# Kernel optimization log

Measured on AMD Instinct MI355X. Metric: run time of the kernel, lower is better.

## Reference

```python
import jax, jax.numpy as jnp
import numpy as np

NUM_NODES = 50000
NUM_RELATIONS = 16
HIDDEN = 128
NUM_LAYERS = 3
NUM_EDGES = 1600000


def setup_inputs() -> dict:
    key = jax.random.key(0)
    ks = jax.random.split(key, 6)
    edge_index = jax.random.randint(ks[0], (2, NUM_EDGES), 0, NUM_NODES, dtype=jnp.int64)
    edge_type = jax.random.randint(ks[1], (NUM_EDGES,), 0, NUM_RELATIONS, dtype=jnp.int64)
    scale = 1.0 / np.sqrt(HIDDEN)
    node_init = jax.random.normal(ks[2], (NUM_NODES, HIDDEN), dtype=jnp.float32) * scale
    W = jax.random.normal(ks[3], (NUM_LAYERS, NUM_RELATIONS, HIDDEN, HIDDEN), dtype=jnp.float32) * scale
    root = jax.random.normal(ks[4], (NUM_LAYERS, HIDDEN, HIDDEN), dtype=jnp.float32) * scale
    bias = jnp.zeros((NUM_LAYERS, HIDDEN), dtype=jnp.float32)
    return {"edge_index": edge_index, "edge_type": edge_type,
            "node_init": node_init, "W": W, "root": root, "bias": bias}


def _fast_rgcn_layer(x, src, tgt, edge_type, W_r, root_r, bias_r):
    # FastRGCNConv with aggr='mean': mean of messages per (target node, relation),
    # message = x_src @ W[relation]. By linearity, aggregate normalized x_src per
    # (node, relation) first, then apply relation weights with a single einsum.
    N, d = x.shape
    R = W_r.shape[0]
    seg = tgt * R + edge_type                       # combined (node, relation) segment id
    msg = x[src]                                    # [E, d] irregular gather
    agg = jax.ops.segment_sum(msg, seg, num_segments=N * R).reshape(N, R, d)
    cnt = jax.ops.segment_sum(jnp.ones_like(edge_type, dtype=x.dtype), seg,
                              num_segments=N * R).reshape(N, R, 1)
    agg = agg / jnp.clip(cnt, 1.0, None)            # per-(node,relation) mean
    out = jnp.einsum('nrd,rdo->no', agg, W_r)       # relation-specific transform
    out = out + x @ root_r + bias_r                 # root/self connection + bias
    return out


def reference(edge_index, edge_type, node_init, W, root, bias):
    src, tgt = edge_index[0], edge_index[1]
    x = node_init
    for i in range(NUM_LAYERS):
        x = _fast_rgcn_layer(x, src, tgt, edge_type, W[i], root[i], bias[i])
        if i < NUM_LAYERS - 1:
            x = jax.nn.relu(x)  # dropout omitted (eval mode)
    return x
```

## Files before the change

kernel.cpp:

```cpp
#include <hip/hip_runtime.h>
#include <hip/hip_bf16.h>

#define N_NODES   50000
#define N_REL     16
#define HID       128
#define N_EDGES   1600000
#define N_TILES   3125
#define N_BINS    800000
#define N_RUNS    50000
#define N_SCANBLK 49
#define N_MBLK    1563
#define PAYLOAD_CAP 2400064
#define BS_LAYER  278528
#define AG_STRIDE 136

typedef unsigned short ushort_t;
typedef __attribute__((ext_vector_type(8))) short short8;
typedef __attribute__((ext_vector_type(4))) float f32x4;

union BF2U { __hip_bfloat162 h; unsigned u; };

__device__ __forceinline__ unsigned pack_bf16_2(float x, float y) {
  BF2U c; c.h = __float22bfloat162_rn(make_float2(x, y));
  return c.u;
}

__device__ __forceinline__ void lds_barrier() {
  asm volatile("s_waitcnt lgkmcnt(0)\n\ts_barrier" ::: "memory");
}


__global__ __launch_bounds__(256) void k_hist(const int* __restrict__ ei,
                                              const int* __restrict__ et,
                                              int* __restrict__ cnt,
                                              int* __restrict__ rank) {
  int e = blockIdx.x * 256 + threadIdx.x;
  int tgt = ei[N_EDGES + e];
  int r   = et[e];
  int key = ((tgt >> 4) << 8) | (r << 4) | (tgt & 15);
  rank[e] = atomicAdd(&cnt[key], 1);
}

__global__ __launch_bounds__(256) void k_runpad(const int* __restrict__ cnt,
                                                int* __restrict__ padtot) {
  int r = blockIdx.x * 256 + threadIdx.x;
  if (r >= N_RUNS) return;
  const int4* c4 = (const int4*)(cnt + r * 16);
  int s = 0;
#pragma unroll
  for (int j = 0; j < 4; ++j) { int4 v = c4[j]; s += v.x + v.y + v.z + v.w; }
  padtot[r] = (s + 15) & ~15;
}

__global__ __launch_bounds__(256) void k_btot(const int* __restrict__ in,
                                              int* __restrict__ totals, int n) {
  __shared__ int s[256];
  int t = threadIdx.x, b = blockIdx.x;
  int sum = 0;
  for (int j = 0; j < 4; ++j) {
    int idx = b * 1024 + j * 256 + t;
    sum += (idx < n) ? in[idx] : 0;
  }
  s[t] = sum; __syncthreads();
  for (int ofs = 128; ofs > 0; ofs >>= 1) {
    if (t < ofs) s[t] += s[t + ofs];
    __syncthreads();
  }
  if (t == 0) totals[b] = s[0];
}

__global__ __launch_bounds__(1024) void k_scan_totals(int* totals, int* endp, int nblk) {
  __shared__ int s[1024];
  int t = threadIdx.x;
  int v = (t < nblk) ? totals[t] : 0;
  s[t] = v; __syncthreads();
  for (int ofs = 1; ofs < 1024; ofs <<= 1) {
    int x = (t >= ofs) ? s[t - ofs] : 0;
    __syncthreads();
    s[t] += x;
    __syncthreads();
  }
  if (t < nblk) totals[t] = s[t] - v;
  if (t == nblk - 1) *endp = s[t];
}

__global__ __launch_bounds__(1024) void k_scan_within(int* __restrict__ a,
                                                      const int* __restrict__ totals,
                                                      int n) {
  __shared__ int s[1024];
  int t = threadIdx.x, blk = blockIdx.x;
  int b = blk * 1024 + t;
  int v = (b < n) ? a[b] : 0;
  s[t] = v; __syncthreads();
  for (int ofs = 1; ofs < 1024; ofs <<= 1) {
    int x = (t >= ofs) ? s[t - ofs] : 0;
    __syncthreads();
    s[t] += x;
    __syncthreads();
  }
  if (b < n) a[b] = totals[blk] + s[t] - v;
}

__global__ __launch_bounds__(256) void k_fineoff(const int* __restrict__ cnt,
                                                 const int* __restrict__ run_start,
                                                 int* __restrict__ fine_start,
                                                 unsigned* __restrict__ payload) {
  int r = blockIdx.x * 256 + threadIdx.x;
  if (r >= N_RUNS) return;
  int base = run_start[r];
  int e1   = run_start[r + 1];
  int pfx = 0;
  for (int i = 0; i < 16; ++i) {
    fine_start[r * 16 + i] = base + pfx;
    pfx += cnt[r * 16 + i];
  }
  const unsigned dummy = ((unsigned)N_NODES << 16) | (1u << 4) | 15u;
  for (int j = base + pfx; j < e1; ++j) payload[j] = dummy;
}

__global__ __launch_bounds__(256) void k_sort(const int* __restrict__ ei,
                                              const int* __restrict__ et,
                                              const int* __restrict__ cnt,
                                              const int* __restrict__ fine_start,
                                              const int* __restrict__ rank,
                                              unsigned* __restrict__ payload) {
  int e = blockIdx.x * 256 + threadIdx.x;
  int src = ei[e];
  int tgt = ei[N_EDGES + e];
  int r   = et[e];
  int key = ((tgt >> 4) << 8) | (r << 4) | (tgt & 15);
  int c = cnt[key]; c = c > 4095 ? 4095 : c;
  int pos = fine_start[key] + rank[e];
  payload[pos] = ((unsigned)src << 16) | ((unsigned)c << 4) | (unsigned)(tgt & 15);
}

__global__ __launch_bounds__(256) void k_bt(const float* __restrict__ W,
                                            const float* __restrict__ root,
                                            ushort_t* __restrict__ Bs) {
  int idx = blockIdx.x * 256 + threadIdx.x;
  int lane = idx & 63;
  int fl   = idx >> 6;
  int frag = fl % 544;
  int l    = fl / 544;
  int cb = frag & 7, kk = (frag >> 3) & 3, r = frag >> 5;
  int col = cb * 16 + (lane & 15);
  int d0  = kk * 32 + (lane >> 4) * 8;
  const float* srcp = (r < 16)
      ? W + ((size_t)(l * N_REL + r) * HID + d0) * HID + col
      : root + ((size_t)l * HID + d0) * HID + col;
  ushort_t out[8];
#pragma unroll
  for (int j = 0; j < 8; ++j) {
    union { __hip_bfloat16 h; ushort_t u; } c;
    c.h = __float2bfloat16(srcp[(size_t)j * HID]);
    out[j] = c.u;
  }
  *(short8*)(Bs + ((size_t)fl << 9) + lane * 8) = *(short8*)out;
}

__global__ __launch_bounds__(256) void k_xh(const float* __restrict__ xin,
                                            ushort_t* __restrict__ xh) {
  int i = blockIdx.x * 256 + threadIdx.x;
  float4 v = ((const float4*)xin)[i];
  uint2 u;
  u.x = pack_bf16_2(v.x, v.y);
  u.y = pack_bf16_2(v.z, v.w);
  ((uint2*)xh)[i] = u;
}

__global__ __launch_bounds__(256) void k_zrow(ushort_t* xa, ushort_t* xb) {
  int t = threadIdx.x;
  if (t < 128) xa[(size_t)N_NODES * HID + t] = 0;
  else         xb[(size_t)N_NODES * HID + (t - 128)] = 0;
}


__global__ __launch_bounds__(256, 4) void k_main(const ushort_t* __restrict__ xh,
                                                 ushort_t* __restrict__ xh_out,
                                                 float* __restrict__ fout,
                                                 const ushort_t* __restrict__ Bs,
                                                 const float* __restrict__ bias,
                                                 const int* __restrict__ run_start,
                                                 const unsigned* __restrict__ payload,
                                                 int write_f32) {
  __shared__ alignas(16) ushort_t agg[2][2][32][AG_STRIDE];

  const int tile0 = blockIdx.x * 2;
  const int tid   = threadIdx.x;
  const int wave  = tid >> 6;
  const int lane  = tid & 63;
  const int m16   = lane & 15;
  const int q     = lane >> 4;
  const unsigned* xh32 = (const unsigned*)xh;

  if (wave < 2) {
    const int p = wave;
    int ebv = 0;
    {
      int s8 = lane >> 2, t2 = (lane >> 1) & 1, h = lane & 1;
      int tt = tile0 + t2;
      int idx = (tt < N_TILES) ? (tt * 16 + s8 * 2 + p + h) : N_RUNS;
      if (lane < 32) ebv = run_start[idx];
    }

#define ISSUE16(DST, PV, JB)                                                  \
    _Pragma("unroll")                                                         \
    for (int k1 = 0; k1 < 16; ++k1) {                                         \
      unsigned spq = (unsigned)__builtin_amdgcn_readlane(PV, (JB) + k1);      \
      DST[k1] = xh32[(spq >> 16) * 64 + lane];                                \
    }

#define FLUSHM(TB, BUF)                                                       \
    if (mcur >= 0) {                                                          \
      float sc = __builtin_amdgcn_rcpf((float)scnt);                          \
      *(unsigned*)&agg[BUF][p][(TB) + mcur][lane * 2] =                       \
          pack_bf16_2(a0 * sc, a1 * sc);                                      \
    }

#define CONSUME1(SPK, XV, TB, BUF)                                            \
    {                                                                         \
      int mk = (int)((SPK) & 15u);                                            \
      if (mk != mcur) {                                                       \
        FLUSHM(TB, BUF);                                                      \
        mcur = mk; scnt = (int)(((SPK) >> 4) & 4095u);                        \
        a0 = 0.f; a1 = 0.f;                                                   \
      }                                                                       \
      a0 += __uint_as_float((XV) << 16);                                      \
      a1 += __uint_as_float((XV) & 0xffff0000u);                              \
    }

#define CONS16(PV, JB, SLOT, TB, BUF)                                         \
    _Pragma("unroll")                                                         \
    for (int k2 = 0; k2 < 16; ++k2) {                                         \
      unsigned spk = (unsigned)__builtin_amdgcn_readlane(PV, (JB) + k2);      \
      CONSUME1(spk, SLOT[k2], TB, BUF);                                       \
    }

#define RUNX(PV, E0, E1, CNT, B0, B1, TB)                                     \
    {                                                                         \
      int mcur = -1, scnt = 1;                                                \
      float a0 = 0.f, a1 = 0.f;                                               \
      if ((CNT) > 0) {                                                        \
        CONS16(PV, 0, B0, TB, buf);                                           \
        if ((CNT) > 16) {                                                     \
          CONS16(PV, 16, B1, TB, buf);                                        \
          if ((CNT) > 32) {                                                   \
            CONS16(PV, 32, xqE, TB, buf);                                     \
            if ((CNT) > 48) {                                                 \
              ISSUE16(xqE, PV, 48);                                           \
              CONS16(PV, 48, xqE, TB, buf);                                   \
            }                                                                 \
          }                                                                   \
        }                                                                     \
        for (int c0 = (E0) + 64; c0 < (E1); c0 += 16) {        \
          int pvx = (int)payload[c0 + lane];                                  \
          ISSUE16(xqE, pvx, 0);                                               \
          CONS16(pvx, 0, xqE, TB, buf);                                       \
        }                                                                     \
        FLUSHM(TB, buf);                                                      \
      }                                                                       \
    }

    unsigned xqA[16], xqB[16], xqC[16], xqD[16], xqE[16];

    int e00 = __builtin_amdgcn_readlane(ebv, 0);
    int e01 = __builtin_amdgcn_readlane(ebv, 1);
    int e10 = __builtin_amdgcn_readlane(ebv, 2);
    int e11 = __builtin_amdgcn_readlane(ebv, 3);
    int pv0 = (int)payload[e00 + lane];
    int pv1 = (int)payload[e10 + lane];
    ISSUE16(xqA, pv0, 0);
    ISSUE16(xqC, pv1, 0);

    for (int s = 0; s < 8; ++s) {
      const int buf = s & 1;
      int cnt0 = e01 - e00, cnt1 = e11 - e10;

      if (cnt0 > 16) ISSUE16(xqB, pv0, 16);
      if (cnt1 > 16) ISSUE16(xqD, pv1, 16);
      if (cnt0 > 32) ISSUE16(xqE, pv0, 32);

      int f00 = e00, f01 = e01, f10 = e10, f11 = e11;
      int pvn0 = pv0, pvn1 = pv1;
      if (s < 7) {
        f00 = __builtin_amdgcn_readlane(ebv, (s + 1) * 4 + 0);
        f01 = __builtin_amdgcn_readlane(ebv, (s + 1) * 4 + 1);
        f10 = __builtin_amdgcn_readlane(ebv, (s + 1) * 4 + 2);
        f11 = __builtin_amdgcn_readlane(ebv, (s + 1) * 4 + 3);
        pvn0 = (int)payload[f00 + lane];
        pvn1 = (int)payload[f10 + lane];
      }

      {
        short8 z = {0, 0, 0, 0, 0, 0, 0, 0};
#pragma unroll
        for (int i = 0; i < 8; ++i)
          *(short8*)&agg[buf][p][i * 4 + q][m16 * 8] = z;
      }

      RUNX(pv0, e00, e01, cnt0, xqA, xqB, 0);
      if (cnt1 > 32) ISSUE16(xqE, pv1, 32);
      RUNX(pv1, e10, e11, cnt1, xqC, xqD, 16);

      if (s < 7) {
        e00 = f00; e01 = f01; e10 = f10; e11 = f11;
        pv0 = pvn0; pv1 = pvn1;
        ISSUE16(xqA, pv0, 0);
        ISSUE16(xqC, pv1, 0);
      }
      lds_barrier();
    }
#undef RUNX
#undef CONS16
#undef CONSUME1
#undef FLUSHM
#undef ISSUE16
    return;
  }

  const int c = wave - 2;
  f32x4 acc[2][4];
#pragma unroll
  for (int t = 0; t < 2; ++t)
#pragma unroll
    for (int i = 0; i < 4; ++i) acc[t][i] = (f32x4){0.f, 0.f, 0.f, 0.f};

  for (int s = 0; s < 8; ++s) {
    lds_barrier();
#pragma unroll
    for (int rp = 0; rp < 2; ++rp) {
      int rel = s * 2 + rp;
      short8 Bf[4][4];
#pragma unroll
      for (int kk = 0; kk < 4; ++kk)
#pragma unroll
        for (int i = 0; i < 4; ++i)
          Bf[kk][i] = *(const short8*)(Bs +
              ((size_t)((rel * 4 + kk) * 8 + (c * 4 + i)) << 9) + lane * 8);
#pragma unroll
      for (int kk = 0; kk < 4; ++kk) {
        short8 A0 = *(const short8*)&agg[s & 1][rp][m16][kk * 32 + q * 8];
        short8 A1 = *(const short8*)&agg[s & 1][rp][16 + m16][kk * 32 + q * 8];
#pragma unroll
        for (int i = 0; i < 4; ++i) {
          acc[0][i] = __builtin_amdgcn_mfma_f32_16x16x32_bf16(A0, Bf[kk][i], acc[0][i], 0, 0, 0);
          acc[1][i] = __builtin_amdgcn_mfma_f32_16x16x32_bf16(A1, Bf[kk][i], acc[1][i], 0, 0, 0);
        }
      }
    }
  }

  {
    short8 Bf[4][4];
#pragma unroll
    for (int kk = 0; kk < 4; ++kk)
#pragma unroll
      for (int i = 0; i < 4; ++i)
        Bf[kk][i] = *(const short8*)(Bs +
            ((size_t)((16 * 4 + kk) * 8 + (c * 4 + i)) << 9) + lane * 8);
    int r0 = tile0 * 16 + m16;      if (r0 > N_NODES) r0 = N_NODES;
    int r1 = tile0 * 16 + 16 + m16; if (r1 > N_NODES) r1 = N_NODES;
#pragma unroll
    for (int kk = 0; kk < 4; ++kk) {
      short8 A0 = *(const short8*)(xh + (size_t)r0 * HID + kk * 32 + q * 8);
      short8 A1 = *(const short8*)(xh + (size_t)r1 * HID + kk * 32 + q * 8);
#pragma unroll
      for (int i = 0; i < 4; ++i) {
        acc[0][i] = __builtin_amdgcn_mfma_f32_16x16x32_bf16(A0, Bf[kk][i], acc[0][i], 0, 0, 0);
        acc[1][i] = __builtin_amdgcn_mfma_f32_16x16x32_bf16(A1, Bf[kk][i], acc[1][i], 0, 0, 0);
      }
    }
  }

  float bvv[4];
#pragma unroll
  for (int i = 0; i < 4; ++i) bvv[i] = bias[(c * 4 + i) * 16 + m16];
  int rbase = tile0 * 16 + q * 4;
#pragma unroll
  for (int t = 0; t < 2; ++t)
#pragma unroll
    for (int rg = 0; rg < 4; ++rg) {
      int row = rbase + t * 16 + rg;
      if (row < N_NODES) {
#pragma unroll
        for (int i = 0; i < 4; ++i) {
          float v = acc[t][i][rg] + bvv[i];
          int col = (c * 4 + i) * 16 + m16;
          if (write_f32) {
            fout[(size_t)row * HID + col] = v;
          } else {
            v = fmaxf(v, 0.f);
            union { __hip_bfloat16 h; ushort_t u; } cv;
            cv.h = __float2bfloat16(v);
            xh_out[(size_t)row * HID + col] = cv.u;
          }
        }
      }
    }
}


extern "C" void kernel_launch(void* const* d_in, const int* in_sizes, int n_in,
                              void* d_out, int out_size, void* d_ws, size_t ws_size,
                              hipStream_t stream) {
  const int*   ei        = (const int*)d_in[0];
  const int*   et        = (const int*)d_in[1];
  const float* node_init = (const float*)d_in[2];
  const float* W         = (const float*)d_in[3];
  const float* root      = (const float*)d_in[4];
  const float* bias      = (const float*)d_in[5];
  float* outp = (float*)d_out;

  char* ws = (char*)d_ws;
  size_t o = 0;
  auto carve = [&](size_t bytes) { char* p = ws + o; o = (o + bytes + 255) & ~(size_t)255; return p; };
  ushort_t* xh_a       = (ushort_t*)carve((size_t)(N_NODES + 1) * HID * 2);
  ushort_t* xh_b       = (ushort_t*)carve((size_t)(N_NODES + 1) * HID * 2);
  unsigned* payload    = (unsigned*)carve((size_t)PAYLOAD_CAP * 4);
  int*      cnt        = (int*)     carve((size_t)N_BINS * 4);
  int*      fine_start = (int*)     carve((size_t)N_BINS * 4);
  int*      rank       = (int*)     carve((size_t)N_EDGES * 4);
  int*      run_start  = (int*)     carve((size_t)(N_RUNS + 1) * 4);
  int*      totals     = (int*)     carve((size_t)N_SCANBLK * 4);
  ushort_t* Bs         = (ushort_t*)carve((size_t)3 * BS_LAYER * 2);
  (void)ws_size; (void)n_in; (void)in_sizes; (void)out_size;

  hipMemsetAsync(cnt, 0, (size_t)N_BINS * 4, stream);
  hipLaunchKernelGGL(k_hist,        dim3(N_EDGES / 256), dim3(256), 0, stream, ei, et, cnt, rank);
  hipLaunchKernelGGL(k_runpad,      dim3((N_RUNS + 255) / 256), dim3(256), 0, stream, cnt, run_start);
  hipLaunchKernelGGL(k_btot,        dim3(N_SCANBLK), dim3(256), 0, stream, run_start, totals, N_RUNS);
  hipLaunchKernelGGL(k_scan_totals, dim3(1), dim3(1024), 0, stream, totals, run_start + N_RUNS, N_SCANBLK);
  hipLaunchKernelGGL(k_scan_within, dim3(N_SCANBLK), dim3(1024), 0, stream, run_start, totals, N_RUNS);
  hipLaunchKernelGGL(k_fineoff,     dim3((N_RUNS + 255) / 256), dim3(256), 0, stream, cnt, run_start, fine_start, payload);
  hipLaunchKernelGGL(k_sort,        dim3(N_EDGES / 256), dim3(256), 0, stream, ei, et, cnt, fine_start, rank, payload);
  hipLaunchKernelGGL(k_bt,          dim3(3 * 544 * 64 / 256), dim3(256), 0, stream, W, root, Bs);
  hipLaunchKernelGGL(k_xh,          dim3(N_NODES * HID / 4 / 256), dim3(256), 0, stream, node_init, xh_a);
  hipLaunchKernelGGL(k_zrow,        dim3(1), dim3(256), 0, stream, xh_a, xh_b);

  hipLaunchKernelGGL(k_main, dim3(N_MBLK), dim3(256), 0, stream,
                     xh_a, xh_b, (float*)nullptr,
                     Bs + (size_t)0 * BS_LAYER, bias + 0 * HID, run_start, payload, 0);
  hipLaunchKernelGGL(k_main, dim3(N_MBLK), dim3(256), 0, stream,
                     xh_b, xh_a, (float*)nullptr,
                     Bs + (size_t)1 * BS_LAYER, bias + 1 * HID, run_start, payload, 0);
  hipLaunchKernelGGL(k_main, dim3(N_MBLK), dim3(256), 0, stream,
                     xh_a, (ushort_t*)nullptr, outp,
                     Bs + (size_t)2 * BS_LAYER, bias + 2 * HID, run_start, payload, 1);
}
```

Before: 611.7 us.

## Fuse preprocessing scan kernels, add sched barriers, lower k_main occupancy bound

Merges run padding with block totals, merges the within-block scan with fine offset computation and dummy padding, and folds the zero-row writes into the bf16 conversion kernel. This cuts the preprocessing launches from nine to six and removes some global round trips. Separately, it inserts sched_barrier fences in the aggregation waves of k_main so the compiler keeps the issue/consume order, and changes launch_bounds from 4 to 3 blocks per CU, which allows more registers per thread but may lower occupancy.

Measured after the change: 611.9 us. About the same (+0.0%).

```diff
diff --git a/kernel.cpp b/kernel.cpp
--- a/kernel.cpp
+++ b/kernel.cpp
@@ -41,32 +41,27 @@
   rank[e] = atomicAdd(&cnt[key], 1);
 }
 
-__global__ __launch_bounds__(256) void k_runpad(const int* __restrict__ cnt,
-                                                int* __restrict__ padtot) {
-  int r = blockIdx.x * 256 + threadIdx.x;
-  if (r >= N_RUNS) return;
-  const int4* c4 = (const int4*)(cnt + r * 16);
-  int s = 0;
-#pragma unroll
-  for (int j = 0; j < 4; ++j) { int4 v = c4[j]; s += v.x + v.y + v.z + v.w; }
-  padtot[r] = (s + 15) & ~15;
-}
-
-__global__ __launch_bounds__(256) void k_btot(const int* __restrict__ in,
-                                              int* __restrict__ totals, int n) {
-  __shared__ int s[256];
-  int t = threadIdx.x, b = blockIdx.x;
-  int sum = 0;
-  for (int j = 0; j < 4; ++j) {
-    int idx = b * 1024 + j * 256 + t;
-    sum += (idx < n) ? in[idx] : 0;
-  }
-  s[t] = sum; __syncthreads();
-  for (int ofs = 128; ofs > 0; ofs >>= 1) {
+__global__ __launch_bounds__(1024) void k_runpad_btot(const int* __restrict__ cnt,
+                                                      int* __restrict__ run_start,
+                                                      int* __restrict__ totals) {
+  __shared__ int s[1024];
+  int t = threadIdx.x, blk = blockIdx.x;
+  int r = blk * 1024 + t;
+  int v = 0;
+  if (r < N_RUNS) {
+    const int4* c4 = (const int4*)(cnt + r * 16);
+    int sum = 0;
+#pragma unroll
+    for (int j = 0; j < 4; ++j) { int4 w = c4[j]; sum += w.x + w.y + w.z + w.w; }
+    v = (sum + 15) & ~15;
+    run_start[r] = v;
+  }
+  s[t] = v; __syncthreads();
+  for (int ofs = 512; ofs > 0; ofs >>= 1) {
     if (t < ofs) s[t] += s[t + ofs];
     __syncthreads();
   }
-  if (t == 0) totals[b] = s[0];
+  if (t == 0) totals[blk] = s[0];
 }
 
 __global__ __launch_bounds__(1024) void k_scan_totals(int* totals, int* endp, int nblk) {
@@ -84,13 +79,15 @@
   if (t == nblk - 1) *endp = s[t];
 }
 
-__global__ __launch_bounds__(1024) void k_scan_within(int* __restrict__ a,
-                                                      const int* __restrict__ totals,
-                                                      int n) {
+__global__ __launch_bounds__(1024) void k_scan_fineoff(int* __restrict__ run_start,
+                                                       const int* __restrict__ totals,
+                                                       const int* __restrict__ cnt,
+                                                       int* __restrict__ fine_start,
+                                                       unsigned* __restrict__ payload) {
   __shared__ int s[1024];
   int t = threadIdx.x, blk = blockIdx.x;
-  int b = blk * 1024 + t;
-  int v = (b < n) ? a[b] : 0;
+  int r = blk * 1024 + t;
+  int v = (r < N_RUNS) ? run_start[r] : 0;
   s[t] = v; __syncthreads();
   for (int ofs = 1; ofs < 1024; ofs <<= 1) {
     int x = (t >= ofs) ? s[t - ofs] : 0;
@@ -98,24 +95,18 @@
     s[t] += x;
     __syncthreads();
   }
-  if (b < n) a[b] = totals[blk] + s[t] - v;
-}
-
-__global__ __launch_bounds__(256) void k_fineoff(const int* __restrict__ cnt,
-                                                 const int* __restrict__ run_start,
-                                                 int* __restrict__ fine_start,
-                                                 unsigned* __restrict__ payload) {
-  int r = blockIdx.x * 256 + threadIdx.x;
-  if (r >= N_RUNS) return;
-  int base = run_start[r];
-  int e1   = run_start[r + 1];
-  int pfx = 0;
-  for (int i = 0; i < 16; ++i) {
-    fine_start[r * 16 + i] = base + pfx;
-    pfx += cnt[r * 16 + i];
-  }
-  const unsigned dummy = ((unsigned)N_NODES << 16) | (1u << 4) | 15u;
-  for (int j = base + pfx; j < e1; ++j) payload[j] = dummy;
+  if (r < N_RUNS) {
+    int base = totals[blk] + s[t] - v;
+    run_start[r] = base;
+    int pfx = 0;
+#pragma unroll 4
+    for (int i = 0; i < 16; ++i) {
+      fine_start[r * 16 + i] = base + pfx;
+      pfx += cnt[r * 16 + i];
+    }
+    const unsigned dummy = ((unsigned)N_NODES << 16) | (1u << 4) | 15u;
+    for (int j = base + pfx; j < base + v; ++j) payload[j] = dummy;
+  }
 }
 
 __global__ __launch_bounds__(256) void k_sort(const int* __restrict__ ei,
@@ -159,23 +150,24 @@
 }
 
 __global__ __launch_bounds__(256) void k_xh(const float* __restrict__ xin,
-                                            ushort_t* __restrict__ xh) {
+                                            ushort_t* __restrict__ xh_a,
+                                            ushort_t* __restrict__ xh_b) {
   int i = blockIdx.x * 256 + threadIdx.x;
   float4 v = ((const float4*)xin)[i];
   uint2 u;
   u.x = pack_bf16_2(v.x, v.y);
   u.y = pack_bf16_2(v.z, v.w);
-  ((uint2*)xh)[i] = u;
-}
-
-__global__ __launch_bounds__(256) void k_zrow(ushort_t* xa, ushort_t* xb) {
-  int t = threadIdx.x;
-  if (t < 128) xa[(size_t)N_NODES * HID + t] = 0;
-  else         xb[(size_t)N_NODES * HID + (t - 128)] = 0;
-}
-
-
-__global__ __launch_bounds__(256, 4) void k_main(const ushort_t* __restrict__ xh,
+  ((uint2*)xh_a)[i] = u;
+  if (blockIdx.x == 0 && threadIdx.x < 64) {
+    uint2 z = {0u, 0u};
+    ushort_t* dst = (threadIdx.x < 32) ? xh_a : xh_b;
+    int k = threadIdx.x & 31;
+    *(uint2*)(dst + (size_t)N_NODES * HID + k * 4) = z;
+  }
+}
+
+
+__global__ __launch_bounds__(256, 3) void k_main(const ushort_t* __restrict__ xh,
                                                  ushort_t* __restrict__ xh_out,
                                                  float* __restrict__ fout,
                                                  const ushort_t* __restrict__ Bs,
@@ -271,6 +263,7 @@
     int pv1 = (int)payload[e10 + lane];
     ISSUE16(xqA, pv0, 0);
     ISSUE16(xqC, pv1, 0);
+    __builtin_amdgcn_sched_barrier(0);
 
     for (int s = 0; s < 8; ++s) {
       const int buf = s & 1;
@@ -290,6 +283,7 @@
         pvn0 = (int)payload[f00 + lane];
         pvn1 = (int)payload[f10 + lane];
       }
+      __builtin_amdgcn_sched_barrier(0);
 
       {
         short8 z = {0, 0, 0, 0, 0, 0, 0, 0};
@@ -300,6 +294,7 @@
 
       RUNX(pv0, e00, e01, cnt0, xqA, xqB, 0);
       if (cnt1 > 32) ISSUE16(xqE, pv1, 32);
+      __builtin_amdgcn_sched_barrier(0);
       RUNX(pv1, e10, e11, cnt1, xqC, xqD, 16);
 
       if (s < 7) {
@@ -308,6 +303,7 @@
         ISSUE16(xqA, pv0, 0);
         ISSUE16(xqC, pv1, 0);
       }
+      __builtin_amdgcn_sched_barrier(0);
       lds_barrier();
     }
 #undef RUNX
@@ -426,16 +422,13 @@
   (void)ws_size; (void)n_in; (void)in_sizes; (void)out_size;
 
   hipMemsetAsync(cnt, 0, (size_t)N_BINS * 4, stream);
-  hipLaunchKernelGGL(k_hist,        dim3(N_EDGES / 256), dim3(256), 0, stream, ei, et, cnt, rank);
-  hipLaunchKernelGGL(k_runpad,      dim3((N_RUNS + 255) / 256), dim3(256), 0, stream, cnt, run_start);
-  hipLaunchKernelGGL(k_btot,        dim3(N_SCANBLK), dim3(256), 0, stream, run_start, totals, N_RUNS);
-  hipLaunchKernelGGL(k_scan_totals, dim3(1), dim3(1024), 0, stream, totals, run_start + N_RUNS, N_SCANBLK);
-  hipLaunchKernelGGL(k_scan_within, dim3(N_SCANBLK), dim3(1024), 0, stream, run_start, totals, N_RUNS);
-  hipLaunchKernelGGL(k_fineoff,     dim3((N_RUNS + 255) / 256), dim3(256), 0, stream, cnt, run_start, fine_start, payload);
-  hipLaunchKernelGGL(k_sort,        dim3(N_EDGES / 256), dim3(256), 0, stream, ei, et, cnt, fine_start, rank, payload);
-  hipLaunchKernelGGL(k_bt,          dim3(3 * 544 * 64 / 256), dim3(256), 0, stream, W, root, Bs);
-  hipLaunchKernelGGL(k_xh,          dim3(N_NODES * HID / 4 / 256), dim3(256), 0, stream, node_init, xh_a);
-  hipLaunchKernelGGL(k_zrow,        dim3(1), dim3(256), 0, stream, xh_a, xh_b);
+  hipLaunchKernelGGL(k_hist,         dim3(N_EDGES / 256), dim3(256), 0, stream, ei, et, cnt, rank);
+  hipLaunchKernelGGL(k_runpad_btot,  dim3(N_SCANBLK), dim3(1024), 0, stream, cnt, run_start, totals);
+  hipLaunchKernelGGL(k_scan_totals,  dim3(1), dim3(1024), 0, stream, totals, run_start + N_RUNS, N_SCANBLK);
+  hipLaunchKernelGGL(k_scan_fineoff, dim3(N_SCANBLK), dim3(1024), 0, stream, run_start, totals, cnt, fine_start, payload);
+  hipLaunchKernelGGL(k_sort,         dim3(N_EDGES / 256), dim3(256), 0, stream, ei, et, cnt, fine_start, rank, payload);
+  hipLaunchKernelGGL(k_bt,           dim3(3 * 544 * 64 / 256), dim3(256), 0, stream, W, root, Bs);
+  hipLaunchKernelGGL(k_xh,           dim3(N_NODES * HID / 4 / 256), dim3(256), 0, stream, node_init, xh_a, xh_b);
 
   hipLaunchKernelGGL(k_main, dim3(N_MBLK), dim3(256), 0, stream,
                      xh_a, xh_b, (float*)nullptr,
```
